# Performance work log

Hardware: AMD Instinct MI355X
Metric: run time of the kernel (lower is better)

## Reference

```python
import jax, jax.numpy as jnp
import numpy as np

EPS = 1e-5

def _instance_norm(t):
    # torch .var(dim=2) default is unbiased (ddof=1) over flattened HW
    b, c, h, w = t.shape
    flat = t.reshape(b, c, h * w)
    mean = flat.mean(axis=2)
    var = flat.var(axis=2, ddof=1) + EPS
    return (t - mean[:, :, None, None]) / jnp.sqrt(var)[:, :, None, None]

def _conv1x1(t, w, b):
    # w: [Cout, Cin], b: [Cout]; t: [B, Cin, H, W]
    return jnp.einsum('oc,bchw->bohw', w, t) + b[None, :, None, None]


def setup_inputs() -> dict:
    key = jax.random.key(0)
    ks = jax.random.split(key, 11)
    B, C, H, W = 4, 512, 64, 64
    scale = 1.0 / np.sqrt(C)
    inp = {
        'c': jax.random.normal(ks[0], (B, C, H, W), jnp.float32),
        's': jax.random.normal(ks[1], (B, C, H, W), jnp.float32),
        'x': jax.random.normal(ks[2], (B, C, H, W), jnp.float32),
        'c_w': jax.random.normal(ks[3], (C, C), jnp.float32) * scale,
        'c_b': jax.random.normal(ks[4], (C,), jnp.float32) * 0.01,
        's_w': jax.random.normal(ks[5], (C, C), jnp.float32) * scale,
        's_b': jax.random.normal(ks[6], (C,), jnp.float32) * 0.01,
        'i_w': jax.random.normal(ks[7], (C, C), jnp.float32) * scale,
        'i_b': jax.random.normal(ks[8], (C,), jnp.float32) * 0.01,
        'o_w': jax.random.normal(ks[9], (C, C), jnp.float32) * scale,
        'o_b': jax.random.normal(ks[10], (C,), jnp.float32) * 0.01,
    }
    return inp


def reference(c, s, x, c_w, c_b, s_w, s_b, i_w, i_b, o_w, o_b):
    B, C, H, W = c.shape
    N = H * W
    cf = _conv1x1(_instance_norm(c), c_w, c_b).reshape(B, C, N)
    sf = _conv1x1(_instance_norm(s), s_w, s_b).reshape(B, C, N)
    xf = _conv1x1(s, i_w, i_b).reshape(B, C, N)
    # mask[b, n, m] = sum_c cf[b, c, n] * sf[b, c, m]; softmax over m
    mask = jax.nn.softmax(jnp.einsum('bcn,bcm->bnm', cf, sf), axis=-1)
    # of = xf @ mask^T : of[b, c, n] = sum_m xf[b, c, m] * mask[b, n, m]
    of = jnp.einsum('bcm,bnm->bcn', xf, mask).reshape(B, C, H, W)
    of = _conv1x1(of, o_w, o_b)
    return x + of
```

## Files before the change

### kernel.cpp

```cpp
#include <hip/hip_runtime.h>

typedef unsigned short u16;
typedef _Float16 f16x8 __attribute__((ext_vector_type(8)));
typedef float f32x4 __attribute__((ext_vector_type(4)));
typedef u16 u16x4 __attribute__((ext_vector_type(4)));
typedef u16 u16x8v __attribute__((ext_vector_type(8)));

__device__ __forceinline__ u16 f2h(float f) {
    _Float16 h = (_Float16)f;
    return __builtin_bit_cast(u16, h);
}
__device__ __forceinline__ float h2f(u16 u) {
    return (float)__builtin_bit_cast(_Float16, u);
}

__global__ void __launch_bounds__(256) stats_kernel(
    const float* __restrict__ c, const float* __restrict__ s,
    float* __restrict__ mC, float* __restrict__ rC,
    float* __restrict__ mS, float* __restrict__ rS)
{
    const float* src = (blockIdx.y ? s : c) + (size_t)blockIdx.x * 4096;
    int t = threadIdx.x, lane = t & 63, wv = t >> 6;
    const float4* p = (const float4*)src;
    float sum = 0.f, sq = 0.f;
#pragma unroll
    for (int i = 0; i < 4; ++i) {
        float4 v = p[t + 256 * i];
        sum += v.x + v.y + v.z + v.w;
        sq  += v.x * v.x + v.y * v.y + v.z * v.z + v.w * v.w;
    }
#pragma unroll
    for (int m = 1; m < 64; m <<= 1) {
        sum += __shfl_xor(sum, m);
        sq  += __shfl_xor(sq, m);
    }
    __shared__ float sa[4], sb[4];
    if (!lane) { sa[wv] = sum; sb[wv] = sq; }
    __syncthreads();
    if (t == 0) {
        float S = sa[0] + sa[1] + sa[2] + sa[3];
        float Q = sb[0] + sb[1] + sb[2] + sb[3];
        float mean = S * (1.0f / 4096.0f);
        float var = (Q - 4096.0f * mean * mean) * (1.0f / 4095.0f);
        float rstd = rsqrtf(var + 1e-5f);
        if (blockIdx.y) { mS[blockIdx.x] = mean; rS[blockIdx.x] = rstd; }
        else            { mC[blockIdx.x] = mean; rC[blockIdx.x] = rstd; }
    }
}

__global__ void __launch_bounds__(256) packall(
    const float* __restrict__ c, const float* __restrict__ s,
    const float* __restrict__ mC, const float* __restrict__ rC,
    const float* __restrict__ mS, const float* __restrict__ rS,
    u16* __restrict__ cnT, u16* __restrict__ snT, u16* __restrict__ sRT)
{
    __shared__ float tile[32][33];
    int z = blockIdx.z;
    bool isS = z >= 4;
    int b = isS ? z - 4 : z;
    const float* src  = isS ? s : c;
    const float* mean = isS ? mS : mC;
    const float* rstd = isS ? rS : rC;
    u16* dh = isS ? snT : cnT;
    int n0 = blockIdx.x * 32, c0 = blockIdx.y * 32;
    int tx = threadIdx.x, ty = threadIdx.y;
    const float* sbp = src + ((size_t)b * 512 + c0) * 4096 + n0;
#pragma unroll
    for (int it = 0; it < 4; ++it) {
        int cc = ty + it * 8;
        tile[cc][tx] = sbp[(size_t)cc * 4096 + tx];
    }
    __syncthreads();
    int ch = c0 + tx;
    float mn = mean[b * 512 + ch];
    float rs = rstd[b * 512 + ch];
    size_t obase = ((size_t)b * 4096 + n0) * 512 + c0;
#pragma unroll
    for (int it = 0; it < 4; ++it) {
        int r = ty + it * 8;
        float v = tile[tx][r];
        size_t o = obase + (size_t)r * 512 + tx;
        dh[o] = f2h((v - mn) * rs);
        if (isS) sRT[o] = f2h(v);
    }
}

__global__ void __launch_bounds__(256) prep_kernel(
    const float* __restrict__ c_w, const float* __restrict__ s_w,
    const float* __restrict__ i_w, const float* __restrict__ o_w,
    u16* __restrict__ cwT, u16* __restrict__ swT,
    u16* __restrict__ iwT, u16* __restrict__ ow)
{
    int z = blockIdx.z;
    int tx = threadIdx.x, ty = threadIdx.y;
    if (z == 3) {
        size_t base = ((size_t)(blockIdx.y * 16 + blockIdx.x) * 256 +
                       (ty * 32 + tx)) * 4;
        float4 v = *(const float4*)(o_w + base);
        u16x4 o;
        o[0] = f2h(v.x); o[1] = f2h(v.y); o[2] = f2h(v.z); o[3] = f2h(v.w);
        *(u16x4*)(ow + base) = o;
        return;
    }
    const float* w = (z == 0) ? c_w : (z == 1) ? s_w : i_w;
    u16* wT = (z == 0) ? cwT : (z == 1) ? swT : iwT;
    __shared__ float tile[32][33];
    int c0 = blockIdx.x * 32, k0 = blockIdx.y * 32;
#pragma unroll
    for (int it = 0; it < 4; ++it) {
        int kk = ty + it * 8;
        tile[kk][tx] = w[(size_t)(k0 + kk) * 512 + c0 + tx];
    }
    __syncthreads();
#pragma unroll
    for (int it = 0; it < 4; ++it) {
        int r = ty + it * 8;
        wT[(size_t)(c0 + r) * 512 + k0 + tx] = f2h(tile[tx][r]);
    }
}

__global__ void __launch_bounds__(256) bias_prep(
    const float* __restrict__ o_w, const float* __restrict__ i_b,
    const float* __restrict__ o_b, const float* __restrict__ s_w,
    const float* __restrict__ c_b, float* __restrict__ v,
    float* __restrict__ wu)
{
    __shared__ float buf[512];
    int t = threadIdx.x;
    bool isWu = blockIdx.x >= 2;
    const float* vec = isWu ? c_b : i_b;
    buf[t] = vec[t]; buf[t + 256] = vec[t + 256];
    __syncthreads();
    int o = (blockIdx.x & 1) * 256 + t;
    if (!isWu) {
        float acc = o_b[o];
        const float* row = o_w + (size_t)o * 512;
        for (int k = 0; k < 512; ++k) acc += row[k] * buf[k];
        v[o] = acc;
    } else {
        float acc = 0.f;
        for (int k = 0; k < 512; ++k) acc += buf[k] * s_w[(size_t)k * 512 + o];
        wu[o] = acc;
    }
}

__global__ void __launch_bounds__(256) rowdot_kernel(
    const u16* __restrict__ snT, const float* __restrict__ wu,
    float* __restrict__ u)
{
    __shared__ float swu[512];
    int t = threadIdx.x;
    swu[t] = wu[t]; swu[t + 256] = wu[t + 256];
    __syncthreads();
    int lane = t & 63, wv = t >> 6;
    int row = blockIdx.x * 4 + wv;
    u16x8v h = *(const u16x8v*)(snT + (size_t)row * 512 + lane * 8);
    float acc = 0.f;
#pragma unroll
    for (int i = 0; i < 8; ++i) acc += h2f(h[i]) * swu[lane * 8 + i];
#pragma unroll
    for (int m = 1; m < 64; m <<= 1) acc += __shfl_xor(acc, m);
    if (!lane) u[row] = acc;
}

#define EPI_F32       0
#define EPI_PLAIN_F16 2

__device__ __forceinline__ void stage_tile(
    const u16* __restrict__ g, int ldk, int i0, int k0, char* tile, int wv, int lane)
{
#pragma unroll
    for (int cc = 0; cc < 4; ++cc) {
        int chunk = (wv * 4 + cc) * 64 + lane;
        int row  = chunk >> 3;
        int slot = chunk & 7;
        int gc   = slot ^ (row & 7);
        const u16* gp = g + (size_t)(i0 + row) * ldk + (k0 + gc * 8);
        char* lp = tile + (size_t)(wv * 4 + cc) * 1024;
        __builtin_amdgcn_global_load_lds(
            (const __attribute__((address_space(1))) unsigned int*)gp,
            (__attribute__((address_space(3))) unsigned int*)lp, 16, 0, 0);
    }
}

template<int EPI>
__global__ void __launch_bounds__(256) gemm_bt(
    const u16* __restrict__ A_, const u16* __restrict__ B_,
    int K, int ldk, const float* __restrict__ bias,
    float* __restrict__ outF_, u16* __restrict__ outH_,
    int ldo, int zdiv,
    long aBatch, long aChunk, long bBatch, long bChunk, long oZ)
{
    __shared__ char smem[32768];
    char* sA = smem;
    char* sB = smem + 16384;

    int bz = blockIdx.z;
    int batch = bz / zdiv, chunk = bz % zdiv;
    const u16* A  = A_ + (size_t)batch * aBatch + (size_t)chunk * aChunk;
    const u16* Bm = B_ + (size_t)batch * bBatch + (size_t)chunk * bChunk;

    int i0 = blockIdx.y * 128, j0 = blockIdx.x * 128;
    int tid = threadIdx.x, lane = tid & 63, wv = tid >> 6;
    int wr = wv >> 1, wc = wv & 1;
    int r15 = lane & 15, h4 = lane >> 4;

    f32x4 zero = {0.f, 0.f, 0.f, 0.f};
    f32x4 acc[4][4];
#pragma unroll
    for (int m = 0; m < 4; ++m)
#pragma unroll
        for (int n = 0; n < 4; ++n) acc[m][n] = zero;

    for (int k0 = 0; k0 < K; k0 += 64) {
        stage_tile(A, ldk, i0, k0, sA, wv, lane);
        stage_tile(Bm, ldk, j0, k0, sB, wv, lane);
        asm volatile("s_waitcnt vmcnt(0)" ::: "memory");
        __syncthreads();
#pragma unroll
        for (int ks = 0; ks < 2; ++ks) {
            f16x8 a[4], b[4];
#pragma unroll
            for (int m = 0; m < 4; ++m) {
                int row = wr * 64 + m * 16 + r15;
                int off = row * 128 + (((ks * 4 + h4) ^ (row & 7)) << 4);
                a[m] = *(const f16x8*)(sA + off);
            }
#pragma unroll
            for (int n = 0; n < 4; ++n) {
                int col = wc * 64 + n * 16 + r15;
                int off = col * 128 + (((ks * 4 + h4) ^ (col & 7)) << 4);
                b[n] = *(const f16x8*)(sB + off);
            }
#pragma unroll
            for (int m = 0; m < 4; ++m)
#pragma unroll
                for (int n = 0; n < 4; ++n)
                    acc[m][n] = __builtin_amdgcn_mfma_f32_16x16x32_f16(a[m], b[n], acc[m][n], 0, 0, 0);
        }
        __syncthreads();
    }

    float* outF = outF_ ? outF_ + (size_t)bz * oZ : nullptr;
    u16* outH = outH_ ? outH_ + (size_t)bz * oZ : nullptr;

#pragma unroll
    for (int m = 0; m < 4; ++m)
#pragma unroll
        for (int n = 0; n < 4; ++n) {
            int ibase = i0 + wr * 64 + m * 16 + h4 * 4;
            int j = j0 + wc * 64 + n * 16 + r15;
#pragma unroll
            for (int r = 0; r < 4; ++r) {
                int i = ibase + r;
                float v = acc[m][n][r];
                if constexpr (EPI == EPI_PLAIN_F16) {
                    if (bias) v += bias[i];
                    outH[(size_t)i * ldo + j] = f2h(v);
                } else {
                    outF[(size_t)i * ldo + j] = v;
                }
            }
        }
}

__global__ void __launch_bounds__(256) softmax16(
    u16* __restrict__ LP, const float* __restrict__ u)
{
    u16x8v* row = (u16x8v*)(LP + (size_t)blockIdx.x * 4096);
    const float4* u4 = (const float4*)(u + (size_t)(blockIdx.x >> 12) * 4096);
    int t = threadIdx.x, lane = t & 63, wv = t >> 6;
    u16x8v ca = row[t], cb = row[t + 256];
    float4 ua0 = u4[2 * t], ua1 = u4[2 * t + 1];
    float4 ub0 = u4[2 * (t + 256)], ub1 = u4[2 * (t + 256) + 1];
    float va[8], vb[8];
    va[0] = h2f(ca[0]) + ua0.x; va[1] = h2f(ca[1]) + ua0.y;
    va[2] = h2f(ca[2]) + ua0.z; va[3] = h2f(ca[3]) + ua0.w;
    va[4] = h2f(ca[4]) + ua1.x; va[5] = h2f(ca[5]) + ua1.y;
    va[6] = h2f(ca[6]) + ua1.z; va[7] = h2f(ca[7]) + ua1.w;
    vb[0] = h2f(cb[0]) + ub0.x; vb[1] = h2f(cb[1]) + ub0.y;
    vb[2] = h2f(cb[2]) + ub0.z; vb[3] = h2f(cb[3]) + ub0.w;
    vb[4] = h2f(cb[4]) + ub1.x; vb[5] = h2f(cb[5]) + ub1.y;
    vb[6] = h2f(cb[6]) + ub1.z; vb[7] = h2f(cb[7]) + ub1.w;
    float mx = -3.4e38f;
#pragma unroll
    for (int i = 0; i < 8; ++i) mx = fmaxf(mx, fmaxf(va[i], vb[i]));
#pragma unroll
    for (int m = 1; m < 64; m <<= 1) mx = fmaxf(mx, __shfl_xor(mx, m));
    __shared__ float sM[4], sS[4];
    if (!lane) sM[wv] = mx;
    __syncthreads();
    mx = fmaxf(fmaxf(sM[0], sM[1]), fmaxf(sM[2], sM[3]));
    float sum = 0.f;
#pragma unroll
    for (int i = 0; i < 8; ++i) {
        va[i] = __expf(va[i] - mx);
        vb[i] = __expf(vb[i] - mx);
        sum += va[i] + vb[i];
    }
#pragma unroll
    for (int m = 1; m < 64; m <<= 1) sum += __shfl_xor(sum, m);
    if (!lane) sS[wv] = sum;
    __syncthreads();
    sum = sS[0] + sS[1] + sS[2] + sS[3];
    float inv = 1.0f / sum;
    u16x8v oa, ob;
#pragma unroll
    for (int i = 0; i < 8; ++i) {
        oa[i] = f2h(va[i] * inv);
        ob[i] = f2h(vb[i] * inv);
    }
    row[t] = oa; row[t + 256] = ob;
}

__global__ void __launch_bounds__(256) reduce4resid(
    const u16* __restrict__ part, const float* __restrict__ xr,
    const float* __restrict__ v, float* __restrict__ out)
{
    const size_t PLANE = 2097152;
    int b = blockIdx.y;
    size_t g8 = ((size_t)blockIdx.x * 256 + threadIdx.x) * 8;
    const u16* p0 = part + (size_t)b * 4 * PLANE + g8;
    float acc[8] = {0.f, 0.f, 0.f, 0.f, 0.f, 0.f, 0.f, 0.f};
#pragma unroll
    for (int k = 0; k < 4; ++k) {
        u16x8v h = *(const u16x8v*)(p0 + (size_t)k * PLANE);
#pragma unroll
        for (int i = 0; i < 8; ++i) acc[i] += h2f(h[i]);
    }
    const float4* xv = (const float4*)(xr + (size_t)b * PLANE + g8);
    float4 x0 = xv[0], x1 = xv[1];
    float vc = v[g8 >> 12];
    float4 o0, o1;
    o0.x = acc[0] + x0.x + vc; o0.y = acc[1] + x0.y + vc;
    o0.z = acc[2] + x0.z + vc; o0.w = acc[3] + x0.w + vc;
    o1.x = acc[4] + x1.x + vc; o1.y = acc[5] + x1.y + vc;
    o1.z = acc[6] + x1.z + vc; o1.w = acc[7] + x1.w + vc;
    float4* op = (float4*)(out + (size_t)b * PLANE + g8);
    op[0] = o0; op[1] = o1;
}

extern "C" void kernel_launch(void* const* d_in, const int* in_sizes, int n_in,
                              void* d_out, int out_size, void* d_ws, size_t ws_size,
                              hipStream_t stream)
{
    const float* c   = (const float*)d_in[0];
    const float* s   = (const float*)d_in[1];
    const float* x   = (const float*)d_in[2];
    const float* c_w = (const float*)d_in[3];
    const float* c_b = (const float*)d_in[4];
    const float* s_w = (const float*)d_in[5];
    const float* s_b = (const float*)d_in[6];
    const float* i_w = (const float*)d_in[7];
    const float* i_b = (const float*)d_in[8];
    const float* o_w = (const float*)d_in[9];
    const float* o_b = (const float*)d_in[10];
    float* out = (float*)d_out;
    char* ws = (char*)d_ws;

    const int B = 4, C = 512, N = 4096;
    const size_t NC = (size_t)N * C;
    const size_t W2 = (size_t)C * C;
    const size_t NN = (size_t)N * N;

    size_t off = 0;
    auto alloc = [&](size_t bytes) { size_t o = off; off += (bytes + 255) & ~(size_t)255; return o; };

    size_t o_meanC = alloc((size_t)B * C * 4);
    size_t o_rstdC = alloc((size_t)B * C * 4);
    size_t o_meanS = alloc((size_t)B * C * 4);
    size_t o_rstdS = alloc((size_t)B * C * 4);
    size_t o_cwT = alloc(W2 * 2);
    size_t o_swT = alloc(W2 * 2);
    size_t o_iwT = alloc(W2 * 2);
    size_t o_ow  = alloc(W2 * 2);
    size_t o_G   = alloc(W2 * 2);
    size_t o_W   = alloc(W2 * 2);
    size_t o_v   = alloc((size_t)C * 4);
    size_t o_wu  = alloc((size_t)C * 4);
    size_t o_u   = alloc((size_t)B * N * 4);
    size_t o_cnT = alloc(B * NC * 2);
    size_t o_snT = alloc(B * NC * 2);
    size_t o_sRT = alloc(B * NC * 2);
    size_t o_sgT = alloc(B * NC * 2);
    size_t o_sW  = alloc(B * NC * 2);
    size_t o_P   = alloc(2 * NN * 2);
    size_t o_pt  = alloc(8 * NC * 2);

    if (ws_size < off) {
        hipMemsetAsync(d_out, 0, (size_t)out_size * 4, stream);
        return;
    }

    float* meanC = (float*)(ws + o_meanC);
    float* rstdC = (float*)(ws + o_rstdC);
    float* meanS = (float*)(ws + o_meanS);
    float* rstdS = (float*)(ws + o_rstdS);
    u16* cwT = (u16*)(ws + o_cwT);
    u16* swT = (u16*)(ws + o_swT);
    u16* iwT = (u16*)(ws + o_iwT);
    u16* ow  = (u16*)(ws + o_ow);
    u16* Gf  = (u16*)(ws + o_G);
    u16* Wf  = (u16*)(ws + o_W);
    float* vb = (float*)(ws + o_v);
    float* wu = (float*)(ws + o_wu);
    float* ub = (float*)(ws + o_u);
    u16* cnT = (u16*)(ws + o_cnT);
    u16* snT = (u16*)(ws + o_snT);
    u16* sRT = (u16*)(ws + o_sRT);
    u16* sgT = (u16*)(ws + o_sgT);
    u16* sW  = (u16*)(ws + o_sW);
    u16* Pb  = (u16*)(ws + o_P);
    u16* partH = (u16*)(ws + o_pt);

    stats_kernel<<<dim3(B * C, 2), 256, 0, stream>>>(c, s, meanC, rstdC, meanS, rstdS);
    packall<<<dim3(N / 32, C / 32, 8), dim3(32, 8), 0, stream>>>(
        c, s, meanC, rstdC, meanS, rstdS, cnT, snT, sRT);
    prep_kernel<<<dim3(16, 16, 4), dim3(32, 8), 0, stream>>>(
        c_w, s_w, i_w, o_w, cwT, swT, iwT, ow);
    bias_prep<<<dim3(4), 256, 0, stream>>>(o_w, i_b, o_b, s_w, c_b, vb, wu);
    gemm_bt<EPI_PLAIN_F16><<<dim3(4, 4, 2), 256, 0, stream>>>(
        cwT, swT, 512, 512, nullptr, nullptr, Gf, 512, 1,
        (long)(3 * W2), 0, (long)W2, 0, (long)W2);
    gemm_bt<EPI_PLAIN_F16><<<dim3(4, 32, B), 256, 0, stream>>>(
        snT, Gf, 512, 512, nullptr, nullptr, sgT, 512, 1,
        (long)NC, 0, 0, 0, (long)NC);
    gemm_bt<EPI_PLAIN_F16><<<dim3(32, 4, B), 256, 0, stream>>>(
        Wf, sRT, 512, 512, nullptr, nullptr, sW, 4096, 1,
        0, 0, (long)NC, 0, (long)NC);
    rowdot_kernel<<<dim3(B * N / 4), 256, 0, stream>>>(snT, wu, ub);
    for (int pb0 = 0; pb0 < B; pb0 += 2) {
        gemm_bt<EPI_PLAIN_F16><<<dim3(32, 32, 2), 256, 0, stream>>>(
            cnT + (size_t)pb0 * NC, sgT + (size_t)pb0 * NC,
            512, 512, nullptr, nullptr, Pb, 4096, 1,
            (long)NC, 0, (long)NC, 0, (long)NN);
        softmax16<<<dim3(2 * N), 256, 0, stream>>>(Pb, ub + (size_t)pb0 * N);
        gemm_bt<EPI_PLAIN_F16><<<dim3(32, 4, 8), 256, 0, stream>>>(
            sW + (size_t)pb0 * NC, Pb, 1024, 4096, nullptr,
            nullptr, partH, 4096, 4,
            (long)NC, 1024L, (long)NN, 1024L, (long)NC);
        reduce4resid<<<dim3((int)(NC / 2048), 2), 256, 0, stream>>>(
            partH, x + (size_t)pb0 * NC, vb, out + (size_t)pb0 * NC);
    }
}
```

Measured before the change: 371.8 us.

## Enlarge GEMM tiles to 256x128 with 512 threads and fuse softmax bias into epilogue

The shared GEMM kernel now runs 8 waves per block and computes a 256x128 output tile. The 128-row B tile is staged once and shared by twice as many output rows, which raises operand reuse and halves the number of blocks per GEMM. The per-column bias u is now added in the score GEMM's epilogue through a new jb pointer, so the softmax kernel no longer loads u. The trade-off is fewer, larger blocks with 48 KB of shared memory each, which can lower occupancy and leave the smaller GEMM grids with poor CU utilisation.

Result: faster. 350.6 us (-5.7%).

```diff
diff --git a/kernel.cpp b/kernel.cpp
--- a/kernel.cpp
+++ b/kernel.cpp
@@ -166,7 +166,7 @@
 #define EPI_F32       0
 #define EPI_PLAIN_F16 2
 
-__device__ __forceinline__ void stage_tile(
+__device__ __forceinline__ void stageA(
     const u16* __restrict__ g, int ldk, int i0, int k0, char* tile, int wv, int lane)
 {
 #pragma unroll
@@ -182,25 +182,40 @@
             (__attribute__((address_space(3))) unsigned int*)lp, 16, 0, 0);
     }
 }
+__device__ __forceinline__ void stageB(
+    const u16* __restrict__ g, int ldk, int j0, int k0, char* tile, int wv, int lane)
+{
+#pragma unroll
+    for (int cc = 0; cc < 2; ++cc) {
+        int chunk = (wv * 2 + cc) * 64 + lane;
+        int row  = chunk >> 3;
+        int slot = chunk & 7;
+        int gc   = slot ^ (row & 7);
+        const u16* gp = g + (size_t)(j0 + row) * ldk + (k0 + gc * 8);
+        char* lp = tile + (size_t)(wv * 2 + cc) * 1024;
+        __builtin_amdgcn_global_load_lds(
+            (const __attribute__((address_space(1))) unsigned int*)gp,
+            (__attribute__((address_space(3))) unsigned int*)lp, 16, 0, 0);
+    }
+}
 
 template<int EPI>
-__global__ void __launch_bounds__(256) gemm_bt(
+__global__ void __launch_bounds__(512) gemm_bt(
     const u16* __restrict__ A_, const u16* __restrict__ B_,
     int K, int ldk, const float* __restrict__ bias,
+    const float* __restrict__ jb, long jbZ,
     float* __restrict__ outF_, u16* __restrict__ outH_,
     int ldo, int zdiv,
     long aBatch, long aChunk, long bBatch, long bChunk, long oZ)
 {
-    __shared__ char smem[32768];
-    char* sA = smem;
-    char* sB = smem + 16384;
+    __shared__ char smem[49152];
 
     int bz = blockIdx.z;
     int batch = bz / zdiv, chunk = bz % zdiv;
     const u16* A  = A_ + (size_t)batch * aBatch + (size_t)chunk * aChunk;
     const u16* Bm = B_ + (size_t)batch * bBatch + (size_t)chunk * bChunk;
 
-    int i0 = blockIdx.y * 128, j0 = blockIdx.x * 128;
+    int i0 = blockIdx.y * 256, j0 = blockIdx.x * 128;
     int tid = threadIdx.x, lane = tid & 63, wv = tid >> 6;
     int wr = wv >> 1, wc = wv & 1;
     int r15 = lane & 15, h4 = lane >> 4;
@@ -213,8 +228,8 @@
         for (int n = 0; n < 4; ++n) acc[m][n] = zero;
 
     for (int k0 = 0; k0 < K; k0 += 64) {
-        stage_tile(A, ldk, i0, k0, sA, wv, lane);
-        stage_tile(Bm, ldk, j0, k0, sB, wv, lane);
+        stageA(A, ldk, i0, k0, smem, wv, lane);
+        stageB(Bm, ldk, j0, k0, smem + 32768, wv, lane);
         asm volatile("s_waitcnt vmcnt(0)" ::: "memory");
         __syncthreads();
 #pragma unroll
@@ -224,13 +239,13 @@
             for (int m = 0; m < 4; ++m) {
                 int row = wr * 64 + m * 16 + r15;
                 int off = row * 128 + (((ks * 4 + h4) ^ (row & 7)) << 4);
-                a[m] = *(const f16x8*)(sA + off);
+                a[m] = *(const f16x8*)(smem + off);
             }
 #pragma unroll
             for (int n = 0; n < 4; ++n) {
                 int col = wc * 64 + n * 16 + r15;
                 int off = col * 128 + (((ks * 4 + h4) ^ (col & 7)) << 4);
-                b[n] = *(const f16x8*)(sB + off);
+                b[n] = *(const f16x8*)(smem + 32768 + off);
             }
 #pragma unroll
             for (int m = 0; m < 4; ++m)
@@ -243,6 +258,7 @@
 
     float* outF = outF_ ? outF_ + (size_t)bz * oZ : nullptr;
     u16* outH = outH_ ? outH_ + (size_t)bz * oZ : nullptr;
+    const float* jbp = jb ? jb + (size_t)bz * jbZ : nullptr;
 
 #pragma unroll
     for (int m = 0; m < 4; ++m)
@@ -256,6 +272,7 @@
                 float v = acc[m][n][r];
                 if constexpr (EPI == EPI_PLAIN_F16) {
                     if (bias) v += bias[i];
+                    if (jbp) v += jbp[j];
                     outH[(size_t)i * ldo + j] = f2h(v);
                 } else {
                     outF[(size_t)i * ldo + j] = v;
@@ -264,27 +281,18 @@
         }
 }
 
-__global__ void __launch_bounds__(256) softmax16(
-    u16* __restrict__ LP, const float* __restrict__ u)
+__global__ void __launch_bounds__(256) softmax16(u16* __restrict__ LP)
 {
     u16x8v* row = (u16x8v*)(LP + (size_t)blockIdx.x * 4096);
-    const float4* u4 = (const float4*)(u + (size_t)(blockIdx.x >> 12) * 4096);
     int t = threadIdx.x, lane = t & 63, wv = t >> 6;
     u16x8v ca = row[t], cb = row[t + 256];
-    float4 ua0 = u4[2 * t], ua1 = u4[2 * t + 1];
-    float4 ub0 = u4[2 * (t + 256)], ub1 = u4[2 * (t + 256) + 1];
     float va[8], vb[8];
-    va[0] = h2f(ca[0]) + ua0.x; va[1] = h2f(ca[1]) + ua0.y;
-    va[2] = h2f(ca[2]) + ua0.z; va[3] = h2f(ca[3]) + ua0.w;
-    va[4] = h2f(ca[4]) + ua1.x; va[5] = h2f(ca[5]) + ua1.y;
-    va[6] = h2f(ca[6]) + ua1.z; va[7] = h2f(ca[7]) + ua1.w;
-    vb[0] = h2f(cb[0]) + ub0.x; vb[1] = h2f(cb[1]) + ub0.y;
-    vb[2] = h2f(cb[2]) + ub0.z; vb[3] = h2f(cb[3]) + ub0.w;
-    vb[4] = h2f(cb[4]) + ub1.x; vb[5] = h2f(cb[5]) + ub1.y;
-    vb[6] = h2f(cb[6]) + ub1.z; vb[7] = h2f(cb[7]) + ub1.w;
     float mx = -3.4e38f;
 #pragma unroll
-    for (int i = 0; i < 8; ++i) mx = fmaxf(mx, fmaxf(va[i], vb[i]));
+    for (int i = 0; i < 8; ++i) {
+        va[i] = h2f(ca[i]); vb[i] = h2f(cb[i]);
+        mx = fmaxf(mx, fmaxf(va[i], vb[i]));
+    }
 #pragma unroll
     for (int m = 1; m < 64; m <<= 1) mx = fmaxf(mx, __shfl_xor(mx, m));
     __shared__ float sM[4], sS[4];
@@ -388,7 +396,7 @@
     size_t o_pt  = alloc(8 * NC * 2);
 
     if (ws_size < off) {
-        hipMemsetAsync(d_out, 0, (size_t)out_size * 4, stream);
+        (void)hipMemsetAsync(d_out, 0, (size_t)out_size * 4, stream);
         return;
     }
 
@@ -419,24 +427,25 @@
     prep_kernel<<<dim3(16, 16, 4), dim3(32, 8), 0, stream>>>(
         c_w, s_w, i_w, o_w, cwT, swT, iwT, ow);
     bias_prep<<<dim3(4), 256, 0, stream>>>(o_w, i_b, o_b, s_w, c_b, vb, wu);
-    gemm_bt<EPI_PLAIN_F16><<<dim3(4, 4, 2), 256, 0, stream>>>(
-        cwT, swT, 512, 512, nullptr, nullptr, Gf, 512, 1,
+    gemm_bt<EPI_PLAIN_F16><<<dim3(4, 2, 2), 512, 0, stream>>>(
+        cwT, swT, 512, 512, nullptr, nullptr, 0, nullptr, Gf, 512, 1,
         (long)(3 * W2), 0, (long)W2, 0, (long)W2);
-    gemm_bt<EPI_PLAIN_F16><<<dim3(4, 32, B), 256, 0, stream>>>(
-        snT, Gf, 512, 512, nullptr, nullptr, sgT, 512, 1,
+    gemm_bt<EPI_PLAIN_F16><<<dim3(4, 16, B), 512, 0, stream>>>(
+        snT, Gf, 512, 512, nullptr, nullptr, 0, nullptr, sgT, 512, 1,
         (long)NC, 0, 0, 0, (long)NC);
-    gemm_bt<EPI_PLAIN_F16><<<dim3(32, 4, B), 256, 0, stream>>>(
-        Wf, sRT, 512, 512, nullptr, nullptr, sW, 4096, 1,
+    gemm_bt<EPI_PLAIN_F16><<<dim3(32, 2, B), 512, 0, stream>>>(
+        Wf, sRT, 512, 512, nullptr, nullptr, 0, nullptr, sW, 4096, 1,
         0, 0, (long)NC, 0, (long)NC);
     rowdot_kernel<<<dim3(B * N / 4), 256, 0, stream>>>(snT, wu, ub);
     for (int pb0 = 0; pb0 < B; pb0 += 2) {
-        gemm_bt<EPI_PLAIN_F16><<<dim3(32, 32, 2), 256, 0, stream>>>(
+        gemm_bt<EPI_PLAIN_F16><<<dim3(32, 16, 2), 512, 0, stream>>>(
             cnT + (size_t)pb0 * NC, sgT + (size_t)pb0 * NC,
-            512, 512, nullptr, nullptr, Pb, 4096, 1,
+            512, 512, nullptr, ub + (size_t)pb0 * N, (long)N,
+            nullptr, Pb, 4096, 1,
             (long)NC, 0, (long)NC, 0, (long)NN);
-        softmax16<<<dim3(2 * N), 256, 0, stream>>>(Pb, ub + (size_t)pb0 * N);
-        gemm_bt<EPI_PLAIN_F16><<<dim3(32, 4, 8), 256, 0, stream>>>(
-            sW + (size_t)pb0 * NC, Pb, 1024, 4096, nullptr,
+        softmax16<<<dim3(2 * N), 256, 0, stream>>>(Pb);
+        gemm_bt<EPI_PLAIN_F16><<<dim3(32, 2, 8), 512, 0, stream>>>(
+            sW + (size_t)pb0 * NC, Pb, 1024, 4096, nullptr, nullptr, 0,
             nullptr, partH, 4096, 4,
             (long)NC, 1024L, (long)NN, 1024L, (long)NC);
         reduce4resid<<<dim3((int)(NC / 2048), 2), 256, 0, stream>>>(
```
